# Performance work log

Hardware: AMD Instinct MI355X
Metric: run time of the kernel (lower is better)

The kernel has to match this reference:

```python
import jax, jax.numpy as jnp
import numpy as np

N_HEAD = 16
MASKED_BIAS = -10000.0


def setup_inputs() -> dict:
    key = jax.random.key(0)
    k1, k2, k3 = jax.random.split(key, 3)
    B, S, D = 2, 2048, 1024
    hidden_states = jax.random.normal(k1, (B, S, D), dtype=jnp.float32)
    c_attn_w = jax.random.normal(k2, (D, 3 * D), dtype=jnp.float32) * 0.02
    c_attn_b = jnp.zeros((3 * D,), dtype=jnp.float32)
    c_proj_w = jax.random.normal(k3, (D, D), dtype=jnp.float32) * 0.02
    c_proj_b = jnp.zeros((D,), dtype=jnp.float32)
    return {"hidden_states": hidden_states, "c_attn_w": c_attn_w,
            "c_attn_b": c_attn_b, "c_proj_w": c_proj_w, "c_proj_b": c_proj_b}


def reference(hidden_states, c_attn_w, c_attn_b, c_proj_w, c_proj_b):
    B, S, D = hidden_states.shape
    H = N_HEAD
    hd = D // H
    # Conv1D: x @ W + b, fused QKV
    qkv = hidden_states @ c_attn_w + c_attn_b  # [B, S, 3D]
    q, k, v = jnp.split(qkv, 3, axis=-1)
    # split heads -> [B, H, S, hd]
    q = q.reshape(B, S, H, hd).transpose(0, 2, 1, 3)
    k = k.reshape(B, S, H, hd).transpose(0, 2, 1, 3)
    v = v.reshape(B, S, H, hd).transpose(0, 2, 1, 3)
    # scores with scale=True: divide by sqrt(head_dim)
    w = jnp.einsum('bhqd,bhkd->bhqk', q, k) / jnp.sqrt(jnp.asarray(hd, q.dtype))
    causal = jnp.tril(jnp.ones((S, S), dtype=bool))  # [S, S]
    w = jnp.where(causal[None, None], w, jnp.asarray(MASKED_BIAS, w.dtype))
    w = jax.nn.softmax(w, axis=-1)
    a = jnp.einsum('bhqk,bhkd->bhqd', w, v)
    # merge heads -> [B, S, D]
    a = a.transpose(0, 2, 1, 3).reshape(B, S, D)
    out = a @ c_proj_w + c_proj_b
    return out
```

## Files before the change

kernel.cpp:

```cpp
#include <hip/hip_runtime.h>
#include <hip/hip_bf16.h>
#include <stdint.h>

typedef short short8 __attribute__((ext_vector_type(8)));
typedef short short4v __attribute__((ext_vector_type(4)));
typedef float f32x4 __attribute__((ext_vector_type(4)));

__device__ __forceinline__ unsigned short f2b(float x) {
  __hip_bfloat16 h = __float2bfloat16(x);
  return *reinterpret_cast<unsigned short*>(&h);
}

typedef __attribute__((address_space(1))) const void* gvp_t;
typedef __attribute__((address_space(3))) void* lvp_t;
__device__ __forceinline__ void gl2lds16(const void* g, void* l) {
  __builtin_amdgcn_global_load_lds((gvp_t)g, (lvp_t)l, 16, 0, 0);
}

__global__ void cvt_kernel(const float* __restrict__ in, unsigned short* __restrict__ out, int n4) {
  int i = blockIdx.x * blockDim.x + threadIdx.x;
  if (i >= n4) return;
  const float4 v = reinterpret_cast<const float4*>(in)[i];
  ushort4 o;
  o.x = f2b(v.x); o.y = f2b(v.y); o.z = f2b(v.z); o.w = f2b(v.w);
  reinterpret_cast<ushort4*>(out)[i] = o;
}

__global__ void tpose_kernel(const float* __restrict__ W, unsigned short* __restrict__ Wt,
                             int K, int N) {
  __shared__ float tile[32][33];
  const int nkb = K >> 5;
  const int bk = blockIdx.x % nkb, bn = blockIdx.x / nkb;
  const int k0 = bk * 32, n0 = bn * 32;
  const int tx = threadIdx.x & 31, ty = threadIdx.x >> 5;
#pragma unroll
  for (int i = 0; i < 4; i++) {
    int r = ty + i * 8;
    tile[r][tx] = W[(size_t)(k0 + r) * N + n0 + tx];
  }
  __syncthreads();
#pragma unroll
  for (int i = 0; i < 4; i++) {
    int r = ty + i * 8;
    Wt[(size_t)(n0 + r) * K + k0 + tx] = f2b(tile[tx][r]);
  }
}

__global__ void vtpose_kernel(const unsigned short* __restrict__ Vb, unsigned short* __restrict__ Vt) {
  __shared__ unsigned short t[64][72];
  const int bh = blockIdx.x >> 5;
  const int s0 = (blockIdx.x & 31) * 64;
  const int tid = threadIdx.x;
  const int r = tid >> 3;
  const int c8 = (tid & 7) * 8;
  const unsigned short* src = Vb + ((size_t)bh * 2048 + s0) * 64;
#pragma unroll
  for (int i = 0; i < 2; i++) {
    short8 v = *reinterpret_cast<const short8*>(src + (size_t)(r + i * 32) * 64 + c8);
#pragma unroll
    for (int j = 0; j < 8; j++) t[r + i * 32][c8 + j] = (unsigned short)v[j];
  }
  __syncthreads();
  unsigned short* dst = Vt + (size_t)bh * 64 * 2048 + s0;
#pragma unroll
  for (int i = 0; i < 2; i++) {
    const int d = r + i * 32;
    short8 v;
#pragma unroll
    for (int j = 0; j < 8; j++) v[j] = (short)t[c8 + j][d];
    *reinterpret_cast<short8*>(dst + (size_t)d * 2048 + c8) = v;
  }
}

template<int MODE>
__global__ __launch_bounds__(256)
void gemm_bt(const unsigned short* __restrict__ A, const unsigned short* __restrict__ Bt,
             const float* __restrict__ bias, void* __restrict__ out, int N) {
  constexpr int K = 1024;
  __shared__ __align__(16) unsigned short As[128 * 32];
  __shared__ __align__(16) unsigned short Bs[128 * 32];
  const int nbn = N >> 7;
  const int bm = blockIdx.x / nbn, bn = blockIdx.x % nbn;
  const int tid = threadIdx.x;
  const int lane = tid & 63, wave = tid >> 6;
  const int lo = lane & 15, g = lane >> 4;
  const int wr = (wave >> 1) * 64, wc = (wave & 1) * 64;

  const size_t arow0 = (size_t)bm * 128;
  const size_t brow0 = (size_t)bn * 128;

  f32x4 acc[4][4] = {};

  const int r_a = tid >> 2;
  const int c8 = (tid & 3) * 8;
  const unsigned short* gA0 = A + (arow0 + r_a) * K + c8;
  const unsigned short* gA1 = A + (arow0 + 64 + r_a) * K + c8;
  const unsigned short* gB0 = Bt + (brow0 + r_a) * K + c8;
  const unsigned short* gB1 = Bt + (brow0 + 64 + r_a) * K + c8;
  unsigned short* lA0 = As + wave * 512;
  unsigned short* lA1 = As + 2048 + wave * 512;
  unsigned short* lB0 = Bs + wave * 512;
  unsigned short* lB1 = Bs + 2048 + wave * 512;

  for (int kb = 0; kb < K; kb += 32) {
    __syncthreads();
    gl2lds16(gA0 + kb, lA0);
    gl2lds16(gA1 + kb, lA1);
    gl2lds16(gB0 + kb, lB0);
    gl2lds16(gB1 + kb, lB1);
    __syncthreads();
    short8 af[4], bf[4];
#pragma unroll
    for (int m = 0; m < 4; m++)
      af[m] = *reinterpret_cast<const short8*>(As + (wr + m * 16 + lo) * 32 + g * 8);
#pragma unroll
    for (int n = 0; n < 4; n++)
      bf[n] = *reinterpret_cast<const short8*>(Bs + (wc + n * 16 + lo) * 32 + g * 8);
#pragma unroll
    for (int m = 0; m < 4; m++)
#pragma unroll
      for (int n = 0; n < 4; n++)
        acc[m][n] = __builtin_amdgcn_mfma_f32_16x16x32_bf16(af[m], bf[n], acc[m][n], 0, 0, 0);
  }

#pragma unroll
  for (int m = 0; m < 4; m++) {
#pragma unroll
    for (int n = 0; n < 4; n++) {
      const int col = (int)brow0 + wc + n * 16 + lo;
      const float bv = bias[col];
#pragma unroll
      for (int r = 0; r < 4; r++) {
        const int row = (int)arow0 + wr + m * 16 + g * 4 + r;
        const float v = acc[m][n][r] + bv;
        if (MODE == 0) {
          unsigned short* dst = reinterpret_cast<unsigned short*>(out);
          const int which = col >> 10, rem = col & 1023;
          const int h = rem >> 6, d = rem & 63;
          const int b = row >> 11, s = row & 2047;
          const size_t idx = ((size_t)which * 32 + (size_t)(b * 16 + h)) * 2048 * 64 +
                             (size_t)s * 64 + d;
          dst[idx] = f2b(v);
        } else {
          reinterpret_cast<float*>(out)[(size_t)row * N + col] = v;
        }
      }
    }
  }
}

__global__ __launch_bounds__(256, 4)
void attn_kernel(const unsigned short* __restrict__ Qb, const unsigned short* __restrict__ Kb,
                 const unsigned short* __restrict__ Vt, unsigned short* __restrict__ Ab) {
  constexpr int S = 2048, HD = 64;
  __shared__ __align__(16) unsigned short Ks[2][2][2048];
  __shared__ __align__(16) unsigned short Vs[2][2][2048];
  const int tid = threadIdx.x;
  const int lane = tid & 63, wave = tid >> 6;
  const int lo = lane & 15, g = lane >> 4;
  const int qblk = 31 - (blockIdx.x >> 5);
  const int bh = blockIdx.x & 31;
  const int qbase = qblk * 64 + wave * 16;
  const unsigned short* Qh = Qb + (size_t)bh * S * HD;
  const unsigned short* Kh = Kb + (size_t)bh * S * HD;
  const unsigned short* Vh = Vt + (size_t)bh * HD * S;

  const short8 qf0 = *reinterpret_cast<const short8*>(Qh + (size_t)(qbase + lo) * HD + g * 8);
  const short8 qf1 = *reinterpret_cast<const short8*>(Qh + (size_t)(qbase + lo) * HD + 32 + g * 8);

  const int kr = tid >> 3, ku = tid & 7;
  const unsigned short* kgs = Kh + (size_t)kr * HD + ((ku ^ (kr & 7)) << 3);
  const int vd = tid >> 2, vu = tid & 3;
  const unsigned short* vgs = Vh + (size_t)vd * S + ((vu ^ (vd & 3)) << 3);
  const int woff = wave * 512;

#define STAGE(tt, bb)                                                    \
  { const int k0e = (tt) * 64;                                           \
    gl2lds16(kgs + (size_t)k0e * HD,        &Ks[bb][0][woff]);           \
    gl2lds16(kgs + (size_t)(k0e + 32) * HD, &Ks[bb][1][woff]);           \
    gl2lds16(vgs + k0e,                     &Vs[bb][0][woff]);           \
    gl2lds16(vgs + k0e + 32,                &Vs[bb][1][woff]); }

  const int kswz0 = ((g ^ (lo & 7)) << 3);
  const int kswz1 = (((g + 4) ^ (lo & 7)) << 3);
  const int vsw0 = ((((g >> 1)) ^ (lo & 3)) << 3) + (g & 1) * 4;
  const int vsw1 = ((((g >> 1) + 2) ^ (lo & 3)) << 3) + (g & 1) * 4;

  float mrun = -1e30f, lsum = 0.f;
  f32x4 o0 = {}, o1 = {}, o2 = {}, o3 = {};
  const int q_lane = qbase + lo;
  const int nt = qblk + 1;

  STAGE(0, 0);
  __syncthreads();

  int buf = 0;
  for (int t = 0; t < nt; ++t) {
    if (t + 1 < nt) STAGE(t + 1, buf ^ 1);
#pragma unroll
    for (int sc = 0; sc < 2; ++sc) {
      const unsigned short* Kt = &Ks[buf][sc][0];
      const unsigned short* Vl = &Vs[buf][sc][0];
      const int kk0 = t * 64 + sc * 32;

      const short8 kf00 = *reinterpret_cast<const short8*>(Kt + lo * 64 + kswz0);
      const short8 kf01 = *reinterpret_cast<const short8*>(Kt + lo * 64 + kswz1);
      const short8 kf10 = *reinterpret_cast<const short8*>(Kt + (16 + lo) * 64 + kswz0);
      const short8 kf11 = *reinterpret_cast<const short8*>(Kt + (16 + lo) * 64 + kswz1);

      f32x4 z0 = {0.f, 0.f, 0.f, 0.f}, z1 = {0.f, 0.f, 0.f, 0.f};
      __builtin_amdgcn_s_setprio(1);
      z0 = __builtin_amdgcn_mfma_f32_16x16x32_bf16(kf00, qf0, z0, 0, 0, 0);
      z0 = __builtin_amdgcn_mfma_f32_16x16x32_bf16(kf01, qf1, z0, 0, 0, 0);
      z1 = __builtin_amdgcn_mfma_f32_16x16x32_bf16(kf10, qf0, z1, 0, 0, 0);
      z1 = __builtin_amdgcn_mfma_f32_16x16x32_bf16(kf11, qf1, z1, 0, 0, 0);
      __builtin_amdgcn_s_setprio(0);

      float s[8];
#pragma unroll
      for (int j = 0; j < 8; j++) {
        const int kk = kk0 + ((j >> 2) << 4) + g * 4 + (j & 3);
        const float v = ((j >> 2) ? z1[j & 3] : z0[j & 3]) * 0.125f;
        s[j] = (kk > q_lane) ? -10000.f : v;
      }
      float tmax = s[0];
#pragma unroll
      for (int j = 1; j < 8; j++) tmax = fmaxf(tmax, s[j]);
      tmax = fmaxf(tmax, __shfl_xor(tmax, 16));
      tmax = fmaxf(tmax, __shfl_xor(tmax, 32));
      const float mn = fmaxf(mrun, tmax);
      const float cf = __expf(mrun - mn);
      mrun = mn;
      float ps = 0.f;
      short8 pf;
#pragma unroll
      for (int j = 0; j < 8; j++) {
        const float p = __expf(s[j] - mn);
        ps += p;
        pf[j] = (short)f2b(p);
      }
      lsum = lsum * cf + ps;
#pragma unroll
      for (int r = 0; r < 4; r++) {
        const float cr = __shfl(cf, g * 4 + r);
        o0[r] *= cr; o1[r] *= cr; o2[r] *= cr; o3[r] *= cr;
      }

      short8 vf0, vf1, vf2, vf3;
      {
        short4v a0 = *reinterpret_cast<const short4v*>(Vl + (lo +  0) * 32 + vsw0);
        short4v b0 = *reinterpret_cast<const short4v*>(Vl + (lo +  0) * 32 + vsw1);
        short4v a1 = *reinterpret_cast<const short4v*>(Vl + (lo + 16) * 32 + vsw0);
        short4v b1 = *reinterpret_cast<const short4v*>(Vl + (lo + 16) * 32 + vsw1);
        short4v a2 = *reinterpret_cast<const short4v*>(Vl + (lo + 32) * 32 + vsw0);
        short4v b2 = *reinterpret_cast<const short4v*>(Vl + (lo + 32) * 32 + vsw1);
        short4v a3 = *reinterpret_cast<const short4v*>(Vl + (lo + 48) * 32 + vsw0);
        short4v b3 = *reinterpret_cast<const short4v*>(Vl + (lo + 48) * 32 + vsw1);
        vf0 = __builtin_shufflevector(a0, b0, 0, 1, 2, 3, 4, 5, 6, 7);
        vf1 = __builtin_shufflevector(a1, b1, 0, 1, 2, 3, 4, 5, 6, 7);
        vf2 = __builtin_shufflevector(a2, b2, 0, 1, 2, 3, 4, 5, 6, 7);
        vf3 = __builtin_shufflevector(a3, b3, 0, 1, 2, 3, 4, 5, 6, 7);
      }
      __builtin_amdgcn_s_setprio(1);
      o0 = __builtin_amdgcn_mfma_f32_16x16x32_bf16(pf, vf0, o0, 0, 0, 0);
      o1 = __builtin_amdgcn_mfma_f32_16x16x32_bf16(pf, vf1, o1, 0, 0, 0);
      o2 = __builtin_amdgcn_mfma_f32_16x16x32_bf16(pf, vf2, o2, 0, 0, 0);
      o3 = __builtin_amdgcn_mfma_f32_16x16x32_bf16(pf, vf3, o3, 0, 0, 0);
      __builtin_amdgcn_s_setprio(0);
    }
    __syncthreads();
    buf ^= 1;
  }
#undef STAGE

  lsum += __shfl_xor(lsum, 16);
  lsum += __shfl_xor(lsum, 32);

  const int b = bh >> 4, h = bh & 15;
#pragma unroll
  for (int r = 0; r < 4; r++) {
    const float li = 1.f / __shfl(lsum, g * 4 + r);
    const int srow = qbase + g * 4 + r;
    unsigned short* dst = Ab + ((size_t)b * S + srow) * 1024 + h * 64 + lo;
    dst[0]  = f2b(o0[r] * li);
    dst[16] = f2b(o1[r] * li);
    dst[32] = f2b(o2[r] * li);
    dst[48] = f2b(o3[r] * li);
  }
}

extern "C" void kernel_launch(void* const* d_in, const int* in_sizes, int n_in,
                              void* d_out, int out_size, void* d_ws, size_t ws_size,
                              hipStream_t stream) {
  const float* hs       = (const float*)d_in[0];
  const float* c_attn_w = (const float*)d_in[1];
  const float* c_attn_b = (const float*)d_in[2];
  const float* c_proj_w = (const float*)d_in[3];
  const float* c_proj_b = (const float*)d_in[4];

  char* ws = (char*)d_ws;
  unsigned short* Xb    = (unsigned short*)ws;  ws += (size_t)4096 * 1024 * 2;
  unsigned short* Wqkvt = (unsigned short*)ws;  ws += (size_t)3072 * 1024 * 2;
  unsigned short* Wpt   = (unsigned short*)ws;  ws += (size_t)1024 * 1024 * 2;
  unsigned short* QKV   = (unsigned short*)ws;  ws += (size_t)3 * 32 * 2048 * 64 * 2;
  unsigned short* Ab    = (unsigned short*)ws;  ws += (size_t)4096 * 1024 * 2;

  unsigned short* Qb = QKV;
  unsigned short* Kb = QKV + (size_t)32 * 2048 * 64;
  unsigned short* Vb = QKV + (size_t)2 * 32 * 2048 * 64;
  unsigned short* Vt = Xb;

  cvt_kernel<<<4096, 256, 0, stream>>>(hs, Xb, 4096 * 1024 / 4);
  tpose_kernel<<<(1024 / 32) * (3072 / 32), 256, 0, stream>>>(c_attn_w, Wqkvt, 1024, 3072);
  tpose_kernel<<<(1024 / 32) * (1024 / 32), 256, 0, stream>>>(c_proj_w, Wpt, 1024, 1024);
  gemm_bt<0><<<32 * 24, 256, 0, stream>>>(Xb, Wqkvt, c_attn_b, QKV, 3072);
  vtpose_kernel<<<32 * 32, 256, 0, stream>>>(Vb, Vt);
  attn_kernel<<<32 * 32, 256, 0, stream>>>(Qb, Kb, Vt, Ab);
  gemm_bt<1><<<32 * 8, 256, 0, stream>>>(Ab, Wpt, c_proj_b, d_out, 1024);
}
```

Measured before the change: 212.1 us.

## Fuse prep kernels, double-buffer GEMM LDS, write V transposed from QKV GEMM

Folds the fp32-to-bf16 conversion and the two weight transposes into a single prep launch. Removes the separate V transpose kernel by having the QKV GEMM epilogue write V directly in [d][s] layout. The GEMM main loop now uses double-buffered LDS with a prefetch of the next K tile and raises wave priority around the MFMA block. This trades fewer launches and less global traffic for doubled LDS use and scattered strided 2-byte stores for V.

```diff
diff --git a/kernel.cpp b/kernel.cpp
--- a/kernel.cpp
+++ b/kernel.cpp
@@ -17,20 +17,26 @@
   __builtin_amdgcn_global_load_lds((gvp_t)g, (lvp_t)l, 16, 0, 0);
 }
 
-__global__ void cvt_kernel(const float* __restrict__ in, unsigned short* __restrict__ out, int n4) {
-  int i = blockIdx.x * blockDim.x + threadIdx.x;
-  if (i >= n4) return;
-  const float4 v = reinterpret_cast<const float4*>(in)[i];
-  ushort4 o;
-  o.x = f2b(v.x); o.y = f2b(v.y); o.z = f2b(v.z); o.w = f2b(v.w);
-  reinterpret_cast<ushort4*>(out)[i] = o;
-}
-
-__global__ void tpose_kernel(const float* __restrict__ W, unsigned short* __restrict__ Wt,
-                             int K, int N) {
+__global__ void prep_kernel(const float* __restrict__ hs, unsigned short* __restrict__ Xb,
+                            const float* __restrict__ Wqkv, unsigned short* __restrict__ Wqkvt,
+                            const float* __restrict__ Wp, unsigned short* __restrict__ Wpt) {
   __shared__ float tile[32][33];
-  const int nkb = K >> 5;
-  const int bk = blockIdx.x % nkb, bn = blockIdx.x / nkb;
+  const int bid = blockIdx.x;
+  if (bid < 4096) {
+    const int i = bid * 256 + threadIdx.x;
+    const float4 v = reinterpret_cast<const float4*>(hs)[i];
+    ushort4 o;
+    o.x = f2b(v.x); o.y = f2b(v.y); o.z = f2b(v.z); o.w = f2b(v.w);
+    reinterpret_cast<ushort4*>(Xb)[i] = o;
+    return;
+  }
+  const float* W;
+  unsigned short* Wt;
+  int idx, N;
+  if (bid < 4096 + 3072) { idx = bid - 4096; W = Wqkv; Wt = Wqkvt; N = 3072; }
+  else                   { idx = bid - 7168; W = Wp;   Wt = Wpt;   N = 1024; }
+  const int nkb = 32;
+  const int bk = idx % nkb, bn = idx / nkb;
   const int k0 = bk * 32, n0 = bn * 32;
   const int tx = threadIdx.x & 31, ty = threadIdx.x >> 5;
 #pragma unroll
@@ -42,33 +48,7 @@
 #pragma unroll
   for (int i = 0; i < 4; i++) {
     int r = ty + i * 8;
-    Wt[(size_t)(n0 + r) * K + k0 + tx] = f2b(tile[tx][r]);
-  }
-}
-
-__global__ void vtpose_kernel(const unsigned short* __restrict__ Vb, unsigned short* __restrict__ Vt) {
-  __shared__ unsigned short t[64][72];
-  const int bh = blockIdx.x >> 5;
-  const int s0 = (blockIdx.x & 31) * 64;
-  const int tid = threadIdx.x;
-  const int r = tid >> 3;
-  const int c8 = (tid & 7) * 8;
-  const unsigned short* src = Vb + ((size_t)bh * 2048 + s0) * 64;
-#pragma unroll
-  for (int i = 0; i < 2; i++) {
-    short8 v = *reinterpret_cast<const short8*>(src + (size_t)(r + i * 32) * 64 + c8);
-#pragma unroll
-    for (int j = 0; j < 8; j++) t[r + i * 32][c8 + j] = (unsigned short)v[j];
-  }
-  __syncthreads();
-  unsigned short* dst = Vt + (size_t)bh * 64 * 2048 + s0;
-#pragma unroll
-  for (int i = 0; i < 2; i++) {
-    const int d = r + i * 32;
-    short8 v;
-#pragma unroll
-    for (int j = 0; j < 8; j++) v[j] = (short)t[c8 + j][d];
-    *reinterpret_cast<short8*>(dst + (size_t)d * 2048 + c8) = v;
+    Wt[(size_t)(n0 + r) * 1024 + k0 + tx] = f2b(tile[tx][r]);
   }
 }
 
@@ -77,8 +57,9 @@
 void gemm_bt(const unsigned short* __restrict__ A, const unsigned short* __restrict__ Bt,
              const float* __restrict__ bias, void* __restrict__ out, int N) {
   constexpr int K = 1024;
-  __shared__ __align__(16) unsigned short As[128 * 32];
-  __shared__ __align__(16) unsigned short Bs[128 * 32];
+  constexpr int NT = K / 32;
+  __shared__ __align__(16) unsigned short As[2][128 * 32];
+  __shared__ __align__(16) unsigned short Bs[2][128 * 32];
   const int nbn = N >> 7;
   const int bm = blockIdx.x / nbn, bn = blockIdx.x % nbn;
   const int tid = threadIdx.x;
@@ -97,31 +78,39 @@
   const unsigned short* gA1 = A + (arow0 + 64 + r_a) * K + c8;
   const unsigned short* gB0 = Bt + (brow0 + r_a) * K + c8;
   const unsigned short* gB1 = Bt + (brow0 + 64 + r_a) * K + c8;
-  unsigned short* lA0 = As + wave * 512;
-  unsigned short* lA1 = As + 2048 + wave * 512;
-  unsigned short* lB0 = Bs + wave * 512;
-  unsigned short* lB1 = Bs + 2048 + wave * 512;
-
-  for (int kb = 0; kb < K; kb += 32) {
-    __syncthreads();
-    gl2lds16(gA0 + kb, lA0);
-    gl2lds16(gA1 + kb, lA1);
-    gl2lds16(gB0 + kb, lB0);
-    gl2lds16(gB1 + kb, lB1);
-    __syncthreads();
+  const int woff = wave * 512;
+
+#define GSTAGE(tt, bb)                                        \
+  { const int kb = (tt) * 32;                                 \
+    gl2lds16(gA0 + kb, &As[bb][woff]);                        \
+    gl2lds16(gA1 + kb, &As[bb][2048 + woff]);                 \
+    gl2lds16(gB0 + kb, &Bs[bb][woff]);                        \
+    gl2lds16(gB1 + kb, &Bs[bb][2048 + woff]); }
+
+  GSTAGE(0, 0);
+  __syncthreads();
+
+  int buf = 0;
+  for (int t = 0; t < NT; ++t) {
+    if (t + 1 < NT) GSTAGE(t + 1, buf ^ 1);
     short8 af[4], bf[4];
 #pragma unroll
     for (int m = 0; m < 4; m++)
-      af[m] = *reinterpret_cast<const short8*>(As + (wr + m * 16 + lo) * 32 + g * 8);
+      af[m] = *reinterpret_cast<const short8*>(&As[buf][(wr + m * 16 + lo) * 32 + g * 8]);
 #pragma unroll
     for (int n = 0; n < 4; n++)
-      bf[n] = *reinterpret_cast<const short8*>(Bs + (wc + n * 16 + lo) * 32 + g * 8);
+      bf[n] = *reinterpret_cast<const short8*>(&Bs[buf][(wc + n * 16 + lo) * 32 + g * 8]);
+    __builtin_amdgcn_s_setprio(1);
 #pragma unroll
     for (int m = 0; m < 4; m++)
 #pragma unroll
       for (int n = 0; n < 4; n++)
         acc[m][n] = __builtin_amdgcn_mfma_f32_16x16x32_bf16(af[m], bf[n], acc[m][n], 0, 0, 0);
-  }
+    __builtin_amdgcn_s_setprio(0);
+    __syncthreads();
+    buf ^= 1;
+  }
+#undef GSTAGE
 
 #pragma unroll
   for (int m = 0; m < 4; m++) {
@@ -138,8 +127,11 @@
           const int which = col >> 10, rem = col & 1023;
           const int h = rem >> 6, d = rem & 63;
           const int b = row >> 11, s = row & 2047;
-          const size_t idx = ((size_t)which * 32 + (size_t)(b * 16 + h)) * 2048 * 64 +
-                             (size_t)s * 64 + d;
+          size_t idx;
+          if (which == 2)
+            idx = ((size_t)64 + (size_t)(b * 16 + h)) * 2048 * 64 + (size_t)d * 2048 + s;
+          else
+            idx = ((size_t)which * 32 + (size_t)(b * 16 + h)) * 2048 * 64 + (size_t)s * 64 + d;
           dst[idx] = f2b(v);
         } else {
           reinterpret_cast<float*>(out)[(size_t)row * N + col] = v;
@@ -307,14 +299,10 @@
 
   unsigned short* Qb = QKV;
   unsigned short* Kb = QKV + (size_t)32 * 2048 * 64;
-  unsigned short* Vb = QKV + (size_t)2 * 32 * 2048 * 64;
-  unsigned short* Vt = Xb;
-
-  cvt_kernel<<<4096, 256, 0, stream>>>(hs, Xb, 4096 * 1024 / 4);
-  tpose_kernel<<<(1024 / 32) * (3072 / 32), 256, 0, stream>>>(c_attn_w, Wqkvt, 1024, 3072);
-  tpose_kernel<<<(1024 / 32) * (1024 / 32), 256, 0, stream>>>(c_proj_w, Wpt, 1024, 1024);
+  unsigned short* Vt = QKV + (size_t)2 * 32 * 2048 * 64;
+
+  prep_kernel<<<8192, 256, 0, stream>>>(hs, Xb, c_attn_w, Wqkvt, c_proj_w, Wpt);
   gemm_bt<0><<<32 * 24, 256, 0, stream>>>(Xb, Wqkvt, c_attn_b, QKV, 3072);
-  vtpose_kernel<<<32 * 32, 256, 0, stream>>>(Vb, Vt);
   attn_kernel<<<32 * 32, 256, 0, stream>>>(Qb, Kb, Vt, Ab);
   gemm_bt<1><<<32 * 8, 256, 0, stream>>>(Ab, Wpt, c_proj_b, d_out, 1024);
 }
```

Result: no change. 209.5 us (-1.2%).
